# Kernel optimization log

Hardware: AMD Instinct MI355X
Metric: run time of the kernel (lower is better)

The kernel has to match this reference:

```python
import jax, jax.numpy as jnp
import numpy as np

N, M, FIN, K, NNZ = 16, 20000, 64, 4, 320000


def setup_inputs() -> dict:
    key = jax.random.key(0)
    k1, k2, k3, k4 = jax.random.split(key, 4)
    x = jax.random.normal(k1, (N, M, FIN), dtype=jnp.float32)
    L_vals = jax.random.normal(k2, (K, NNZ), dtype=jnp.float32)
    L_rows = jax.random.randint(k3, (K, NNZ), 0, M, dtype=jnp.int32)
    L_cols = jax.random.randint(k4, (K, NNZ), 0, M, dtype=jnp.int32)
    return {"x": x, "L_vals": L_vals, "L_rows": L_rows, "L_cols": L_cols}


def reference(x, L_vals, L_rows, L_cols):
    n, m, fin = x.shape
    kk = L_vals.shape[0]
    # x0: [M, Fin*N]  (transpose + reshape as in the original call())
    x0 = jnp.transpose(x, (1, 2, 0)).reshape(m, fin * n)

    def spmm_plus_x0(vals, rows, cols):
        # sparse [M,M] @ dense [M, Fin*N] via gather + segment-sum, then + x0
        contrib = vals[:, None] * x0[cols]            # [nnz, Fin*N]
        y = jax.ops.segment_sum(contrib, rows, num_segments=m)
        return y + x0

    x_con = jax.vmap(spmm_plus_x0)(L_vals, L_rows, L_cols)  # [K, M, Fin*N]
    out = x_con.reshape(kk, m, fin, n)
    out = jnp.transpose(out, (3, 1, 2, 0)).reshape(n, m, fin * kk)
    return jax.nn.relu(out)
```

## Files before the change

kernel.cpp:

```cpp
#include <hip/hip_runtime.h>

#define N_    16
#define M_    20000
#define FIN_  64
#define K_    4
#define NNZ_  320000
#define KM_   (K_ * M_)
#define KNNZ_ (K_ * NNZ_)
#define CAP_  64


#define XT_BYTES   ((size_t)M_ * FIN_ * N_ * 2)
#define CNT_BYTES  ((size_t)KM_ * 4)
#define SLOT_BYTES ((size_t)KM_ * CAP_ * 4)
#define WS_A (XT_BYTES + CNT_BYTES + SLOT_BYTES)
#define WS_B (CNT_BYTES + SLOT_BYTES)

__device__ __forceinline__ unsigned bf16bits(float v) {
    unsigned u = __float_as_uint(v);
    return (u + 0x7FFFu + ((u >> 16) & 1u)) & 0xFFFF0000u;
}

__global__ __launch_bounds__(256) void transpose_kernel(const float* __restrict__ x,
                                                        uint4* __restrict__ xt4,
                                                        int* __restrict__ cnt) {
    int gtid = blockIdx.x * 256 + threadIdx.x;
    if (gtid < KM_) cnt[gtid] = 0;

    int wid = threadIdx.x >> 6, f = threadIdx.x & 63;
    int m = blockIdx.x * 4 + wid;
    unsigned h[16];
    #pragma unroll
    for (int n = 0; n < N_; ++n)
        h[n] = bf16bits(x[((size_t)n * M_ + m) * FIN_ + f]) >> 16;
    uint4 A, B;
    A.x = h[0]  | (h[1]  << 16); A.y = h[2]  | (h[3]  << 16);
    A.z = h[4]  | (h[5]  << 16); A.w = h[6]  | (h[7]  << 16);
    B.x = h[8]  | (h[9]  << 16); B.y = h[10] | (h[11] << 16);
    B.z = h[12] | (h[13] << 16); B.w = h[14] | (h[15] << 16);
    xt4[m * 128 + f]      = A;
    xt4[m * 128 + 64 + f] = B;
}

__global__ void bin_kernel(const float* __restrict__ vals,
                           const int*   __restrict__ rows,
                           const int*   __restrict__ cols,
                           int*      __restrict__ cnt,
                           unsigned* __restrict__ slots) {
    int idx = blockIdx.x * blockDim.x + threadIdx.x;
    if (idx >= KNNZ_) return;
    int k = idx / NNZ_;
    int b = k * M_ + rows[idx];
    int rank = atomicAdd(&cnt[b], 1);
    if (rank < CAP_)
        slots[(size_t)b * CAP_ + rank] = bf16bits(vals[idx]) | (unsigned)cols[idx];
}

__device__ __forceinline__ void fma8(float* a, float v, uint4 U) {
    a[0] += v * __uint_as_float(U.x << 16);
    a[1] += v * __uint_as_float(U.x & 0xFFFF0000u);
    a[2] += v * __uint_as_float(U.y << 16);
    a[3] += v * __uint_as_float(U.y & 0xFFFF0000u);
    a[4] += v * __uint_as_float(U.z << 16);
    a[5] += v * __uint_as_float(U.z & 0xFFFF0000u);
    a[6] += v * __uint_as_float(U.w << 16);
    a[7] += v * __uint_as_float(U.w & 0xFFFF0000u);
}

__global__ __launch_bounds__(256) void gather_bf16_kernel(const uint4* __restrict__ xt4,
                                                          const int* __restrict__ cnt,
                                                          const unsigned* __restrict__ slots,
                                                          float4* __restrict__ out4) {
    int wid = threadIdx.x >> 6;
    int f   = threadIdx.x & 63;
    int m   = blockIdx.x * 2 + (wid >> 1);
    int hh  = wid & 1;
    int hofs = hh * 64 + f;

    float acc[K_][8];
    {
        uint4 X = xt4[m * 128 + hofs];
        float xv[8];
        xv[0]=__uint_as_float(X.x<<16); xv[1]=__uint_as_float(X.x&0xFFFF0000u);
        xv[2]=__uint_as_float(X.y<<16); xv[3]=__uint_as_float(X.y&0xFFFF0000u);
        xv[4]=__uint_as_float(X.z<<16); xv[5]=__uint_as_float(X.z&0xFFFF0000u);
        xv[6]=__uint_as_float(X.w<<16); xv[7]=__uint_as_float(X.w&0xFFFF0000u);
        #pragma unroll
        for (int k = 0; k < K_; ++k)
            #pragma unroll
            for (int j = 0; j < 8; ++j) acc[k][j] = xv[j];
    }

    #pragma unroll
    for (int k = 0; k < K_; ++k) {
        int b  = k * M_ + m;
        int cn = cnt[b];
        if (cn > CAP_) cn = CAP_;
        unsigned sl = slots[(size_t)b * CAP_ + f];
        for (int g = 0; g < cn; g += 8) {
            int s[8];
            uint4 u[8];
            #pragma unroll
            for (int i = 0; i < 8; ++i)
                s[i] = (g + i < cn) ? __shfl((int)sl, g + i, 64) : 0;
            #pragma unroll
            for (int i = 0; i < 8; ++i) {
                int c = (int)((unsigned)s[i] & 0xFFFFu);
                u[i] = xt4[c * 128 + hofs];
            }
            #pragma unroll
            for (int i = 0; i < 8; ++i) {
                float v = __uint_as_float((unsigned)s[i] & 0xFFFF0000u);
                fma8(acc[k], v, u[i]);
            }
        }
    }

    #pragma unroll
    for (int j = 0; j < 8; ++j) {
        int n = hh * 8 + j;
        float4 w;
        w.x = fmaxf(acc[0][j], 0.0f);
        w.y = fmaxf(acc[1][j], 0.0f);
        w.z = fmaxf(acc[2][j], 0.0f);
        w.w = fmaxf(acc[3][j], 0.0f);
        out4[((size_t)n * M_ + m) * FIN_ + f] = w;
    }
}

__global__ __launch_bounds__(256) void gather_f32_kernel(const float* __restrict__ x,
                                                         const int* __restrict__ cnt,
                                                         const unsigned* __restrict__ slots,
                                                         float4* __restrict__ out4) {
    int wid = threadIdx.x >> 6;
    int f   = threadIdx.x & 63;
    int m   = blockIdx.x * 4 + wid;

    float acc[K_][N_];
    #pragma unroll
    for (int n = 0; n < N_; ++n) {
        float xv = x[((size_t)n * M_ + m) * FIN_ + f];
        #pragma unroll
        for (int k = 0; k < K_; ++k) acc[k][n] = xv;
    }

    #pragma unroll
    for (int k = 0; k < K_; ++k) {
        int b  = k * M_ + m;
        int cn = cnt[b];
        if (cn > CAP_) cn = CAP_;
        unsigned sl = slots[(size_t)b * CAP_ + f];
        for (int j = 0; j < cn; ++j) {
            int s = __shfl((int)sl, j, 64);
            float v = __uint_as_float((unsigned)s & 0xFFFF0000u);
            int   c = (int)((unsigned)s & 0xFFFFu);
            const float* xp = x + (size_t)c * FIN_ + f;
            #pragma unroll
            for (int n = 0; n < N_; ++n)
                acc[k][n] += v * xp[(size_t)n * (M_ * FIN_)];
        }
    }

    #pragma unroll
    for (int n = 0; n < N_; ++n) {
        float4 w;
        w.x = fmaxf(acc[0][n], 0.0f);
        w.y = fmaxf(acc[1][n], 0.0f);
        w.z = fmaxf(acc[2][n], 0.0f);
        w.w = fmaxf(acc[3][n], 0.0f);
        out4[((size_t)n * M_ + m) * FIN_ + f] = w;
    }
}

__global__ void zero_cnt_kernel(int* __restrict__ cnt) {
    int i = blockIdx.x * blockDim.x + threadIdx.x;
    if (i < KM_) cnt[i] = 0;
}

__global__ void init_out_kernel(const float* __restrict__ x, float* __restrict__ out) {
    int i = blockIdx.x * blockDim.x + threadIdx.x;
    const int tot = N_ * M_ * FIN_;
    if (i < tot) {
        float v = x[i];
        reinterpret_cast<float4*>(out)[i] = make_float4(v, v, v, v);
    }
}

__global__ void scatter_kernel(const float* __restrict__ x,
                               const float* __restrict__ vals,
                               const int*   __restrict__ rows,
                               const int*   __restrict__ cols,
                               float* __restrict__ out) {
    long long idx = (long long)blockIdx.x * blockDim.x + threadIdx.x;
    int f  = (int)(idx & 63);
    int ea = (int)(idx >> 6);
    if (ea >= KNNZ_) return;
    int k = ea / NNZ_;
    float v = vals[ea];
    int r = rows[ea];
    int c = cols[ea];
    const float* xp = x   + (size_t)c * FIN_ + f;
    float*       op = out + ((size_t)r * FIN_ + f) * K_ + k;
    #pragma unroll
    for (int n = 0; n < N_; ++n)
        atomicAdd(op + (size_t)n * (M_ * FIN_ * K_), v * xp[(size_t)n * (M_ * FIN_)]);
}

__global__ void relu_kernel(float* __restrict__ out) {
    int i = blockIdx.x * blockDim.x + threadIdx.x;
    const int tot4 = (N_ * M_ * FIN_ * K_) / 4;
    if (i < tot4) {
        float4 v = reinterpret_cast<float4*>(out)[i];
        v.x = fmaxf(v.x, 0.0f); v.y = fmaxf(v.y, 0.0f);
        v.z = fmaxf(v.z, 0.0f); v.w = fmaxf(v.w, 0.0f);
        reinterpret_cast<float4*>(out)[i] = v;
    }
}

extern "C" void kernel_launch(void* const* d_in, const int* in_sizes, int n_in,
                              void* d_out, int out_size, void* d_ws, size_t ws_size,
                              hipStream_t stream) {
    const float* x    = (const float*)d_in[0];
    const float* vals = (const float*)d_in[1];
    const int*   rows = (const int*)d_in[2];
    const int*   cols = (const int*)d_in[3];
    float*       out  = (float*)d_out;
    char*        ws   = (char*)d_ws;

    if (ws_size >= WS_A) {
        uint4*    xt4   = (uint4*)ws;
        int*      cnt   = (int*)(ws + XT_BYTES);
        unsigned* slots = (unsigned*)(ws + XT_BYTES + CNT_BYTES);

        transpose_kernel<<<M_ / 4, 256, 0, stream>>>(x, xt4, cnt);
        bin_kernel<<<(KNNZ_ + 255) / 256, 256, 0, stream>>>(vals, rows, cols, cnt, slots);
        gather_bf16_kernel<<<M_ / 2, 256, 0, stream>>>(xt4, cnt, slots, (float4*)out);
    } else if (ws_size >= WS_B) {
        int*      cnt   = (int*)ws;
        unsigned* slots = (unsigned*)(ws + CNT_BYTES);

        zero_cnt_kernel<<<(KM_ + 255) / 256, 256, 0, stream>>>(cnt);
        bin_kernel<<<(KNNZ_ + 255) / 256, 256, 0, stream>>>(vals, rows, cols, cnt, slots);
        gather_f32_kernel<<<M_ / 4, 256, 0, stream>>>(x, cnt, slots, (float4*)out);
    } else {
        init_out_kernel<<<(N_ * M_ * FIN_ + 255) / 256, 256, 0, stream>>>(x, out);
        {
            long long tot = (long long)KNNZ_ * 64;
            scatter_kernel<<<(int)((tot + 255) / 256), 256, 0, stream>>>(x, vals, rows, cols, out);
        }
        relu_kernel<<<(N_ * M_ * FIN_ * K_ / 4 + 255) / 256, 256, 0, stream>>>(out);
    }
}
```

Baseline: 485.7 us.

## Split gather work across K per wave and recombine via LDS

The bf16 gather kernel now gives each wave a single k (Chebyshev order) instead of looping over all four inside one wave. Each block handles one (m, half) pair, and results are exchanged through shared memory before the ReLU'd float4 output is written. This shortens the per-wave serial dependency chain, cuts accumulator registers from 32 to 8, and launches four times as many blocks. In exchange it adds an LDS round trip plus a block barrier, and the four waves of a block can have uneven nonzero counts. Addressing also moves to byte-offset shifts.

```diff
diff --git a/kernel.cpp b/kernel.cpp
--- a/kernel.cpp
+++ b/kernel.cpp
@@ -67,63 +67,57 @@
     a[7] += v * __uint_as_float(U.w & 0xFFFF0000u);
 }
 
-__global__ __launch_bounds__(256) void gather_bf16_kernel(const uint4* __restrict__ xt4,
-                                                          const int* __restrict__ cnt,
+__global__ __launch_bounds__(256) void gather_bf16_kernel(const char* __restrict__ xtb,
+                                                          const int* __restrict__ cnt_arr,
                                                           const unsigned* __restrict__ slots,
                                                           float4* __restrict__ out4) {
-    int wid = threadIdx.x >> 6;
-    int f   = threadIdx.x & 63;
-    int m   = blockIdx.x * 2 + (wid >> 1);
-    int hh  = wid & 1;
-    int hofs = hh * 64 + f;
-
-    float acc[K_][8];
+    __shared__ float lds[K_][8][64];
+    int k  = threadIdx.x >> 6;
+    int f  = threadIdx.x & 63;
+    int m  = blockIdx.x >> 1;
+    int hh = blockIdx.x & 1;
+    const char* rowbase = xtb + hh * 1024 + f * 16;
+
+    float acc[8];
     {
-        uint4 X = xt4[m * 128 + hofs];
-        float xv[8];
-        xv[0]=__uint_as_float(X.x<<16); xv[1]=__uint_as_float(X.x&0xFFFF0000u);
-        xv[2]=__uint_as_float(X.y<<16); xv[3]=__uint_as_float(X.y&0xFFFF0000u);
-        xv[4]=__uint_as_float(X.z<<16); xv[5]=__uint_as_float(X.z&0xFFFF0000u);
-        xv[6]=__uint_as_float(X.w<<16); xv[7]=__uint_as_float(X.w&0xFFFF0000u);
+        uint4 X = *(const uint4*)(rowbase + ((size_t)m << 11));
+        acc[0]=__uint_as_float(X.x<<16); acc[1]=__uint_as_float(X.x&0xFFFF0000u);
+        acc[2]=__uint_as_float(X.y<<16); acc[3]=__uint_as_float(X.y&0xFFFF0000u);
+        acc[4]=__uint_as_float(X.z<<16); acc[5]=__uint_as_float(X.z&0xFFFF0000u);
+        acc[6]=__uint_as_float(X.w<<16); acc[7]=__uint_as_float(X.w&0xFFFF0000u);
+    }
+
+    int b  = k * M_ + m;
+    int cn = cnt_arr[b];
+    if (cn > CAP_) cn = CAP_;
+    unsigned sl = slots[(size_t)b * CAP_ + f];
+
+    for (int g = 0; g < cn; g += 8) {
+        uint4 u[8];
+        float v[8];
         #pragma unroll
-        for (int k = 0; k < K_; ++k)
-            #pragma unroll
-            for (int j = 0; j < 8; ++j) acc[k][j] = xv[j];
-    }
-
-    #pragma unroll
-    for (int k = 0; k < K_; ++k) {
-        int b  = k * M_ + m;
-        int cn = cnt[b];
-        if (cn > CAP_) cn = CAP_;
-        unsigned sl = slots[(size_t)b * CAP_ + f];
-        for (int g = 0; g < cn; g += 8) {
-            int s[8];
-            uint4 u[8];
-            #pragma unroll
-            for (int i = 0; i < 8; ++i)
-                s[i] = (g + i < cn) ? __shfl((int)sl, g + i, 64) : 0;
-            #pragma unroll
-            for (int i = 0; i < 8; ++i) {
-                int c = (int)((unsigned)s[i] & 0xFFFFu);
-                u[i] = xt4[c * 128 + hofs];
-            }
-            #pragma unroll
-            for (int i = 0; i < 8; ++i) {
-                float v = __uint_as_float((unsigned)s[i] & 0xFFFF0000u);
-                fma8(acc[k], v, u[i]);
-            }
+        for (int i = 0; i < 8; ++i) {
+            int s = (g + i < cn) ? __shfl((int)sl, g + i, 64) : 0;
+            v[i] = __uint_as_float((unsigned)s & 0xFFFF0000u);
+            u[i] = *(const uint4*)(rowbase + ((size_t)((unsigned)s & 0xFFFFu) << 11));
         }
-    }
-
-    #pragma unroll
-    for (int j = 0; j < 8; ++j) {
+        #pragma unroll
+        for (int i = 0; i < 8; ++i) fma8(acc, v[i], u[i]);
+    }
+
+    #pragma unroll
+    for (int j = 0; j < 8; ++j) lds[k][j][f] = acc[j];
+    __syncthreads();
+
+    #pragma unroll
+    for (int t = 0; t < 2; ++t) {
+        int j = (k << 1) + t;
         int n = hh * 8 + j;
         float4 w;
-        w.x = fmaxf(acc[0][j], 0.0f);
-        w.y = fmaxf(acc[1][j], 0.0f);
-        w.z = fmaxf(acc[2][j], 0.0f);
-        w.w = fmaxf(acc[3][j], 0.0f);
+        w.x = fmaxf(lds[0][j][f], 0.0f);
+        w.y = fmaxf(lds[1][j][f], 0.0f);
+        w.z = fmaxf(lds[2][j][f], 0.0f);
+        w.w = fmaxf(lds[3][j][f], 0.0f);
         out4[((size_t)n * M_ + m) * FIN_ + f] = w;
     }
 }
@@ -234,7 +228,7 @@
 
         transpose_kernel<<<M_ / 4, 256, 0, stream>>>(x, xt4, cnt);
         bin_kernel<<<(KNNZ_ + 255) / 256, 256, 0, stream>>>(vals, rows, cols, cnt, slots);
-        gather_bf16_kernel<<<M_ / 2, 256, 0, stream>>>(xt4, cnt, slots, (float4*)out);
+        gather_bf16_kernel<<<M_ * 2, 256, 0, stream>>>((const char*)ws, cnt, slots, (float4*)out);
     } else if (ws_size >= WS_B) {
         int*      cnt   = (int*)ws;
         unsigned* slots = (unsigned*)(ws + CNT_BYTES);
```

Result: faster. 452.4 us (-6.9%).
